# Kernel optimization log

Hardware: AMD Instinct MI355X
Metric: run time of the kernel (lower is better)

## Reference

```python
import jax, jax.numpy as jnp
import numpy as np

EMBED_DIM = 1024
NUM_HEADS = 16
NUM_GROUPS = 8
HEAD_DIM = EMBED_DIM // NUM_HEADS  # 64
HEADS_PER_GROUP = NUM_HEADS // NUM_GROUPS  # 2
B, S = 4, 2048


def setup_inputs() -> dict:
    key = jax.random.key(0)
    ks = jax.random.split(key, 9)
    init = lambda k, shape: jax.random.normal(k, shape, dtype=jnp.float32) * 0.02
    return {
        "x": jax.random.normal(ks[0], (B, S, EMBED_DIM), dtype=jnp.float32),
        "Wq": init(ks[1], (EMBED_DIM, NUM_GROUPS * HEAD_DIM)),
        "bq": jnp.zeros((NUM_GROUPS * HEAD_DIM,), jnp.float32),
        "Wk": init(ks[2], (EMBED_DIM, EMBED_DIM)),
        "bk": jnp.zeros((EMBED_DIM,), jnp.float32),
        "Wv": init(ks[3], (EMBED_DIM, EMBED_DIM)),
        "bv": jnp.zeros((EMBED_DIM,), jnp.float32),
        "Wo": init(ks[4], (EMBED_DIM, EMBED_DIM)),
        "bo": jnp.zeros((EMBED_DIM,), jnp.float32),
    }


def reference(x, Wq, bq, Wk, bk, Wv, bv, Wo, bo):
    b, s, _ = x.shape
    scale = HEAD_DIM ** -0.5
    # projections
    q = (x @ Wq + bq).reshape(b, s, NUM_GROUPS, HEAD_DIM).transpose(0, 2, 1, 3)   # [b,G,s,d]
    k = (x @ Wk + bk).reshape(b, s, NUM_HEADS, HEAD_DIM).transpose(0, 2, 1, 3)    # [b,H,s,d]
    v = (x @ Wv + bv).reshape(b, s, NUM_HEADS, HEAD_DIM).transpose(0, 2, 1, 3)    # [b,H,s,d]
    # repeat_interleave query groups up to full head count
    q = jnp.repeat(q, HEADS_PER_GROUP, axis=1)                                    # [b,H,s,d]
    scores = jnp.einsum("bhqd,bhkd->bhqk", q, k) * scale                          # [b,H,s,s]
    attn = jax.nn.softmax(scores, axis=-1)
    out = jnp.einsum("bhqk,bhkd->bhqd", attn, v)                                  # [b,H,s,d]
    out = out.transpose(0, 2, 1, 3).reshape(b, s, EMBED_DIM)
    return out @ Wo + bo
```

## Files before the change

kernel.cpp:

```cpp
#include <hip/hip_runtime.h>
#include <hip/hip_bf16.h>
#include <stdint.h>

typedef __bf16 bf16_t;
typedef __bf16 bf16x8 __attribute__((ext_vector_type(8)));
typedef __bf16 bf16x4 __attribute__((ext_vector_type(4)));
typedef float  f32x4  __attribute__((ext_vector_type(4)));
typedef float  f32x16 __attribute__((ext_vector_type(16)));
typedef unsigned int u32x2 __attribute__((ext_vector_type(2)));
typedef unsigned int u32x4 __attribute__((ext_vector_type(4)));

#define B_  4
#define S_  2048
#define H_  16
#define G_  8
#define D_  64

#define QSCALE 0.18033688011112042f
#define SM_BIAS -12.0f

__device__ __forceinline__ void gload_lds16(const bf16_t* g, void* l) {
  __builtin_amdgcn_global_load_lds((const __attribute__((address_space(1))) void*)g,
                                   (__attribute__((address_space(3))) void*)l,
                                   16, 0, 0);
}

__device__ __forceinline__ float fexp2(float x) {
  return __builtin_amdgcn_exp2f(x);
}

__device__ __forceinline__ unsigned cvt_pk(float a, float b) {
  unsigned r;
  asm("v_cvt_pk_bf16_f32 %0, %1, %2" : "=v"(r) : "v"(a), "v"(b));
  return r;
}

__device__ __forceinline__ float xhalf_add(float v) {
  u32x2 r = __builtin_amdgcn_permlane32_swap(__builtin_bit_cast(unsigned, v),
                                             __builtin_bit_cast(unsigned, v), false, false);
  return __builtin_bit_cast(float, r[0]) + __builtin_bit_cast(float, r[1]);
}

__global__ __launch_bounds__(256) void cast_x_kernel(const float* __restrict__ x,
                                                     bf16_t* __restrict__ y) {
  const size_t i = (size_t)blockIdx.x * blockDim.x + threadIdx.x;
  const f32x4* src = (const f32x4*)(x + i * 8);
  f32x4 a = src[0], b = src[1];
  bf16x8 o;
  o[0] = (bf16_t)a[0]; o[1] = (bf16_t)a[1]; o[2] = (bf16_t)a[2]; o[3] = (bf16_t)a[3];
  o[4] = (bf16_t)b[0]; o[5] = (bf16_t)b[1]; o[6] = (bf16_t)b[2]; o[7] = (bf16_t)b[3];
  *(bf16x8*)(y + i * 8) = o;
}

__global__ __launch_bounds__(256) void transpose_cast(const float* __restrict__ W,
                                                      bf16_t* __restrict__ WT,
                                                      int N, int rowOff) {
  __shared__ float tile[64][65];
  const int n0 = blockIdx.x * 64, k0 = blockIdx.y * 64;
  const int tx = threadIdx.x & 63, ty = threadIdx.x >> 6;
  #pragma unroll
  for (int r = ty; r < 64; r += 4)
    tile[r][tx] = W[(size_t)(k0 + r) * N + n0 + tx];
  __syncthreads();
  #pragma unroll
  for (int r = ty; r < 64; r += 4)
    WT[(size_t)(rowOff + n0 + r) * 1024 + k0 + tx] = (bf16_t)tile[tx][r];
}

template<int MODE>
__global__ __launch_bounds__(256) void gemm_bt(
    const bf16_t* __restrict__ A, const bf16_t* __restrict__ BT,
    const float* __restrict__ b0, const float* __restrict__ b1, const float* __restrict__ b2,
    bf16_t* __restrict__ qo, bf16_t* __restrict__ ko, bf16_t* __restrict__ vo,
    float* __restrict__ fout, int N) {
  __shared__ char lds[65536];
  const int tid  = threadIdx.x;
  const int wave = tid >> 6, lane = tid & 63;

  const int nwg  = gridDim.x * gridDim.y;
  const int cpx  = nwg >> 3;
  const int orig = blockIdx.y * gridDim.x + blockIdx.x;
  const int work = (orig & 7) * cpx + (orig >> 3);
  const int bx = work % gridDim.x, by = work / gridDim.x;

  const int bm = by * 128, bn = bx * 128;
  const int wm = (wave >> 1) * 64, wn = (wave & 1) * 64;
  const int l15 = lane & 15;

  const int sg = lane >> 3;
  const int sw = (lane & 7) ^ sg;
  const bf16_t* aSrc = A  + (size_t)(bm + sg) * 1024 + sw * 8;
  const bf16_t* bSrc = BT + (size_t)(bn + sg) * 1024 + sw * 8;

  const char* aAddr[2];
  const char* bAddr[2];
  #pragma unroll
  for (int ks = 0; ks < 2; ++ks) {
    const int slotx = ((ks * 4 + (lane >> 4)) ^ (l15 & 7)) << 4;
    aAddr[ks] = lds + (wm + l15) * 128 + slotx;
    bAddr[ks] = lds + 16384 + (wn + l15) * 128 + slotx;
  }

  f32x4 acc[4][4] = {};

  #define GSTAGE(kt_, SLOT_) do {                                              \
    char* dA_ = lds + (SLOT_) * 32768;                                         \
    char* dB_ = dA_ + 16384;                                                   \
    const int k0_ = (kt_) * 64;                                                \
    _Pragma("unroll")                                                          \
    for (int i_ = 0; i_ < 4; ++i_) {                                           \
      const int c_ = wave * 4 + i_;                                            \
      gload_lds16(aSrc + (size_t)c_ * 8 * 1024 + k0_, dA_ + c_ * 1024);        \
      gload_lds16(bSrc + (size_t)c_ * 8 * 1024 + k0_, dB_ + c_ * 1024);        \
    }                                                                          \
  } while (0)

  #define GWAIT0 do {                                                          \
    asm volatile("s_waitcnt vmcnt(0)" ::: "memory");                           \
    __builtin_amdgcn_s_barrier();                                              \
  } while (0)

  #define COMP(SLOT_) do {                                                     \
    _Pragma("unroll")                                                          \
    for (int ks = 0; ks < 2; ++ks) {                                           \
      bf16x8 af[4], bfr[4];                                                    \
      _Pragma("unroll")                                                        \
      for (int mt = 0; mt < 4; ++mt)                                           \
        af[mt] = *(const bf16x8*)(aAddr[ks] + mt * 2048 + (SLOT_) * 32768);    \
      _Pragma("unroll")                                                        \
      for (int nt = 0; nt < 4; ++nt)                                           \
        bfr[nt] = *(const bf16x8*)(bAddr[ks] + nt * 2048 + (SLOT_) * 32768);   \
      __builtin_amdgcn_s_setprio(1);                                           \
      _Pragma("unroll")                                                        \
      for (int mt = 0; mt < 4; ++mt)                                           \
        _Pragma("unroll")                                                      \
        for (int nt = 0; nt < 4; ++nt)                                         \
          acc[mt][nt] = __builtin_amdgcn_mfma_f32_16x16x32_bf16(af[mt], bfr[nt], acc[mt][nt], 0, 0, 0); \
      __builtin_amdgcn_s_setprio(0);                                           \
    }                                                                          \
  } while (0)

  GSTAGE(0, 0);
  GWAIT0;

  #pragma unroll 1
  for (int u = 0; u < 7; ++u) {
    GSTAGE(2 * u + 1, 1); COMP(0); GWAIT0;
    GSTAGE(2 * u + 2, 0); COMP(1); GWAIT0;
  }
  GSTAGE(15, 1); COMP(0); GWAIT0;
  COMP(1);

  #undef GSTAGE
  #undef GWAIT0
  #undef COMP

  if constexpr (MODE == 0) {
    if (bn >= 1536) {
      __syncthreads();
      #pragma unroll
      for (int nt = 0; nt < 4; ++nt) {
        const int nl = wn + nt * 16 + (lane & 15);
        const float bias = b2[bn - 1536 + nl];
        #pragma unroll
        for (int mt = 0; mt < 4; ++mt) {
          #pragma unroll
          for (int p = 0; p < 2; ++p) {
            const int ml = wm + mt * 16 + ((lane >> 4) << 2) + p * 2;
            unsigned u = cvt_pk(acc[mt][nt][p * 2] + bias, acc[mt][nt][p * 2 + 1] + bias);
            *(unsigned*)(lds + nl * 256 + ((((ml >> 3) ^ (nl & 15))) << 4) + (ml & 7) * 2) = u;
          }
        }
      }
      __syncthreads();
      const int bb = bm >> 11, sbase = bm & 2047;
      const int hv = (bn - 1536) >> 6;
      #pragma unroll
      for (int i = 0; i < 8; ++i) {
        const int nl = wave * 32 + i * 4 + (lane >> 4);
        const int mc = lane & 15;
        bf16x8 v = *(const bf16x8*)(lds + nl * 256 + ((mc ^ (nl & 15)) << 4));
        *(bf16x8*)(vo + (size_t)(bb * 16 + hv + (nl >> 6)) * 131072 +
                   (size_t)(nl & 63) * 2048 + sbase + mc * 8) = v;
      }
    } else {
      #pragma unroll
      for (int nt = 0; nt < 4; ++nt) {
        const int n = bn + wn + nt * 16 + (lane & 15);
        float bias; int region, hh, dd;
        if (n < 512) { region = 0; bias = b0[n];       hh = n >> 6;         dd = n & 63; }
        else         { region = 1; bias = b1[n - 512]; hh = (n - 512) >> 6; dd = (n - 512) & 63; }
        #pragma unroll
        for (int mt = 0; mt < 4; ++mt) {
          #pragma unroll
          for (int r = 0; r < 4; ++r) {
            const int m  = bm + wm + mt * 16 + ((lane >> 4) << 2) + r;
            const int bb = m >> 11, s = m & 2047;
            const float val = acc[mt][nt][r] + bias;
            if (region == 0)
              qo[(size_t)(bb * 8 + hh) * 131072 + s * 64 + dd] = (bf16_t)(val * QSCALE);
            else
              ko[(size_t)(bb * 16 + hh) * 131072 + s * 64 + dd] = (bf16_t)val;
          }
        }
      }
    }
  } else {
    #pragma unroll
    for (int nt = 0; nt < 4; ++nt) {
      const int n = bn + wn + nt * 16 + (lane & 15);
      const float bias = b0[n];
      #pragma unroll
      for (int mt = 0; mt < 4; ++mt) {
        #pragma unroll
        for (int r = 0; r < 4; ++r) {
          const int m = bm + wm + mt * 16 + ((lane >> 4) << 2) + r;
          fout[(size_t)m * 1024 + n] = acc[mt][nt][r] + bias;
        }
      }
    }
  }
}

__global__ __launch_bounds__(256, 2) void attn_kernel(
    const bf16_t* __restrict__ Q, const bf16_t* __restrict__ K,
    const bf16_t* __restrict__ Vt, bf16_t* __restrict__ O) {
  __shared__ char lds[49152];

  const int tid  = threadIdx.x;
  const int wave = tid >> 6, lane = tid & 63;
  const int bh = blockIdx.x;
  const int b = bh >> 4, h = bh & 15, g = h >> 1;
  const int qb = blockIdx.y * 256 + wave * 64;
  const int ql = lane & 31, hi = lane >> 5;
  const int swz = (ql & 7);

  const bf16_t* Qb = Q + ((size_t)(b * G_ + g) * S_ + qb) * D_;
  bf16x8 qf[2][4];
  #pragma unroll
  for (int qg = 0; qg < 2; ++qg)
    #pragma unroll
    for (int ks = 0; ks < 4; ++ks)
      qf[qg][ks] = *(const bf16x8*)(Qb + (size_t)(qg * 32 + ql) * D_ + ks * 16 + hi * 8);

  const char* ab[4];
  #pragma unroll
  for (int i = 0; i < 4; ++i)
    ab[i] = lds + ql * 128 + ((((i << 1) | hi) ^ swz) << 4);

  const int sg = lane >> 3, sw = (lane & 7) ^ sg;
  const int c = wave * 2;
  const bf16_t* kS = K  + (size_t)(b * H_ + h) * S_ * D_ + (size_t)(c * 8 + sg) * D_ + sw * 8;
  const bf16_t* vS = Vt + (size_t)(b * H_ + h) * D_ * S_ + (size_t)(c * 8 + sg) * S_ + sw * 8;

  #define STAGE(t_, SLOT_) do {                                                \
    char* nB = lds + (SLOT_) * 16384;                                          \
    const size_t koff_ = (size_t)(t_) * 64 * D_;                               \
    const size_t voff_ = (size_t)(t_) * 64;                                    \
    gload_lds16(kS + koff_,                 nB + c * 1024);                    \
    gload_lds16(kS + koff_ + 8 * D_,        nB + (c + 1) * 1024);              \
    gload_lds16(vS + voff_,                 nB + 8192 + c * 1024);             \
    gload_lds16(vS + voff_ + 8 * S_,        nB + 8192 + (c + 1) * 1024);       \
  } while (0)

  #define WAIT4 asm volatile("s_waitcnt vmcnt(4)" ::: "memory")
  #define WAIT0 asm volatile("s_waitcnt vmcnt(0)" ::: "memory")

  #define TILE(t_, SLOT_, WAITER_, DOSTAGE_) do {                              \
    WAITER_;                                                                   \
    __builtin_amdgcn_s_barrier();                                              \
    bf16x8 kf[2][4];                                                           \
    _Pragma("unroll")                                                          \
    for (int kg = 0; kg < 2; ++kg)                                             \
      _Pragma("unroll")                                                        \
      for (int ks = 0; ks < 4; ++ks)                                           \
        kf[kg][ks] = *(const bf16x8*)(ab[ks] + kg * 4096 + (SLOT_) * 16384);   \
    u32x4 pf[2][4];                                                            \
    _Pragma("unroll")                                                          \
    for (int qg = 0; qg < 2; ++qg) {                                           \
      f32x16 sc[2];                                                            \
      __builtin_amdgcn_s_setprio(1);                                           \
      sc[0] = __builtin_amdgcn_mfma_f32_32x32x16_bf16(kf[0][0], qf[qg][0], biasv, 0, 0, 0); \
      sc[1] = __builtin_amdgcn_mfma_f32_32x32x16_bf16(kf[1][0], qf[qg][0], biasv, 0, 0, 0); \
      _Pragma("unroll")                                                        \
      for (int ks = 1; ks < 4; ++ks) {                                         \
        sc[0] = __builtin_amdgcn_mfma_f32_32x32x16_bf16(kf[0][ks], qf[qg][ks], sc[0], 0, 0, 0); \
        sc[1] = __builtin_amdgcn_mfma_f32_32x32x16_bf16(kf[1][ks], qf[qg][ks], sc[1], 0, 0, 0); \
      }                                                                        \
      __builtin_amdgcn_s_setprio(0);                                           \
      _Pragma("unroll")                                                        \
      for (int kg = 0; kg < 2; ++kg)                                           \
        _Pragma("unroll")                                                      \
        for (int r = 0; r < 16; ++r)                                           \
          sc[kg][r] = fexp2(sc[kg][r]);                                        \
      lacc[qg] += sc[0];                                                       \
      lacc[qg] += sc[1];                                                       \
      _Pragma("unroll")                                                        \
      for (int kg = 0; kg < 2; ++kg) {                                         \
        _Pragma("unroll")                                                      \
        for (int k2 = 0; k2 < 2; ++k2) {                                       \
          unsigned u0 = cvt_pk(sc[kg][8 * k2 + 0], sc[kg][8 * k2 + 1]);        \
          unsigned u1 = cvt_pk(sc[kg][8 * k2 + 2], sc[kg][8 * k2 + 3]);        \
          unsigned u2 = cvt_pk(sc[kg][8 * k2 + 4], sc[kg][8 * k2 + 5]);        \
          unsigned u3 = cvt_pk(sc[kg][8 * k2 + 6], sc[kg][8 * k2 + 7]);        \
          u32x2 rA = __builtin_amdgcn_permlane32_swap(u0, u2, false, false);   \
          u32x2 rB = __builtin_amdgcn_permlane32_swap(u1, u3, false, false);   \
          u32x4 w; w[0] = rA[0]; w[1] = rB[0]; w[2] = rA[1]; w[3] = rB[1];     \
          pf[qg][kg * 2 + k2] = w;                                             \
        }                                                                      \
      }                                                                        \
    }                                                                          \
    __builtin_amdgcn_s_setprio(1);                                             \
    _Pragma("unroll")                                                          \
    for (int dg = 0; dg < 2; ++dg)                                             \
      _Pragma("unroll")                                                        \
      for (int s4 = 0; s4 < 4; ++s4) {                                         \
        bf16x8 vf = *(const bf16x8*)(ab[s4] + 8192 + dg * 4096 + (SLOT_) * 16384); \
        oacc[0][dg] = __builtin_amdgcn_mfma_f32_32x32x16_bf16(                 \
            vf, __builtin_bit_cast(bf16x8, pf[0][s4]), oacc[0][dg], 0, 0, 0);  \
        oacc[1][dg] = __builtin_amdgcn_mfma_f32_32x32x16_bf16(                 \
            vf, __builtin_bit_cast(bf16x8, pf[1][s4]), oacc[1][dg], 0, 0, 0);  \
      }                                                                        \
    __builtin_amdgcn_s_setprio(0);                                             \
    if (DOSTAGE_) STAGE((t_) + 2, ((SLOT_) + 2) % 3);                          \
  } while (0)

  STAGE(0, 0);
  STAGE(1, 1);

  f32x16 biasv;
  #pragma unroll
  for (int r = 0; r < 16; ++r) biasv[r] = SM_BIAS;

  f32x16 oacc[2][2] = {};
  f32x16 lacc[2] = {};

  #pragma unroll 1
  for (int u = 0; u < 10; ++u) {
    const int t0 = u * 3;
    TILE(t0,     0, WAIT4, 1);
    TILE(t0 + 1, 1, WAIT4, 1);
    TILE(t0 + 2, 2, WAIT4, 1);
  }
  TILE(30, 0, WAIT4, 0);
  TILE(31, 1, WAIT0, 0);

  #undef TILE
  #undef WAIT4
  #undef WAIT0
  #undef STAGE

  #pragma unroll
  for (int qg = 0; qg < 2; ++qg) {
    float l0 = (lacc[qg][0] + lacc[qg][8])  + (lacc[qg][1] + lacc[qg][9]);
    float l1 = (lacc[qg][2] + lacc[qg][10]) + (lacc[qg][3] + lacc[qg][11]);
    float l2 = (lacc[qg][4] + lacc[qg][12]) + (lacc[qg][5] + lacc[qg][13]);
    float l3 = (lacc[qg][6] + lacc[qg][14]) + (lacc[qg][7] + lacc[qg][15]);
    float lst = (l0 + l1) + (l2 + l3);
    lst = xhalf_add(lst);

    const int qrow = qb + qg * 32 + ql;
    const float inv = 1.f / lst;
    bf16_t* ob = O + ((size_t)(b * S_ + qrow) * H_ + h) * D_;
    #pragma unroll
    for (int dg = 0; dg < 2; ++dg) {
      #pragma unroll
      for (int rq = 0; rq < 4; ++rq) {
        bf16x4 o4;
        #pragma unroll
        for (int i = 0; i < 4; ++i)
          o4[i] = (bf16_t)(oacc[qg][dg][rq * 4 + i] * inv);
        *(bf16x4*)(ob + dg * 32 + rq * 8 + hi * 4) = o4;
      }
    }
  }
}

extern "C" void kernel_launch(void* const* d_in, const int* in_sizes, int n_in,
                              void* d_out, int out_size, void* d_ws, size_t ws_size,
                              hipStream_t stream) {
  const float* x  = (const float*)d_in[0];
  const float* Wq = (const float*)d_in[1];
  const float* bq = (const float*)d_in[2];
  const float* Wk = (const float*)d_in[3];
  const float* bk = (const float*)d_in[4];
  const float* Wv = (const float*)d_in[5];
  const float* bv = (const float*)d_in[6];
  const float* Wo = (const float*)d_in[7];
  const float* bo = (const float*)d_in[8];
  (void)in_sizes; (void)n_in; (void)out_size; (void)ws_size;

  char* ws = (char*)d_ws;
  bf16_t* xb  = (bf16_t*)(ws);
  bf16_t* WT  = (bf16_t*)(ws + (16u << 20));
  bf16_t* WoT = (bf16_t*)(ws + (22u << 20));
  bf16_t* q   = (bf16_t*)(ws + (24u << 20));
  bf16_t* kk  = (bf16_t*)(ws + (32u << 20));
  bf16_t* vT  = (bf16_t*)(ws + (48u << 20));
  bf16_t* ao  = (bf16_t*)(ws + (64u << 20));

  cast_x_kernel<<<4096, 256, 0, stream>>>(x, xb);
  transpose_cast<<<dim3(8, 16),  256, 0, stream>>>(Wq, WT, 512, 0);
  transpose_cast<<<dim3(16, 16), 256, 0, stream>>>(Wk, WT, 1024, 512);
  transpose_cast<<<dim3(16, 16), 256, 0, stream>>>(Wv, WT, 1024, 1536);
  transpose_cast<<<dim3(16, 16), 256, 0, stream>>>(Wo, WoT, 1024, 0);
  gemm_bt<0><<<dim3(20, 64), 256, 0, stream>>>(xb, WT, bq, bk, bv, q, kk, vT, nullptr, 2560);
  attn_kernel<<<dim3(64, 8), 256, 0, stream>>>(q, kk, vT, ao);
  gemm_bt<1><<<dim3(8, 64), 256, 0, stream>>>(ao, WoT, bo, nullptr, nullptr, nullptr,
                                              nullptr, nullptr, (float*)d_out, 1024);
}
```

Baseline: 180.3 us.

## Switch attention K/V pipeline to double-buffered two-tile stages with one barrier

```diff
diff --git a/kernel.cpp b/kernel.cpp
--- a/kernel.cpp
+++ b/kernel.cpp
@@ -225,7 +225,7 @@
 __global__ __launch_bounds__(256, 2) void attn_kernel(
     const bf16_t* __restrict__ Q, const bf16_t* __restrict__ K,
     const bf16_t* __restrict__ Vt, bf16_t* __restrict__ O) {
-  __shared__ char lds[49152];
+  __shared__ char lds[65536];
 
   const int tid  = threadIdx.x;
   const int wave = tid >> 6, lane = tid & 63;
@@ -253,28 +253,32 @@
   const bf16_t* kS = K  + (size_t)(b * H_ + h) * S_ * D_ + (size_t)(c * 8 + sg) * D_ + sw * 8;
   const bf16_t* vS = Vt + (size_t)(b * H_ + h) * D_ * S_ + (size_t)(c * 8 + sg) * S_ + sw * 8;
 
-  #define STAGE(t_, SLOT_) do {                                                \
-    char* nB = lds + (SLOT_) * 16384;                                          \
+  #define STAGE2(t_, H_) do {                                                  \
+    char* nB = lds + (H_) * 32768;                                             \
     const size_t koff_ = (size_t)(t_) * 64 * D_;                               \
     const size_t voff_ = (size_t)(t_) * 64;                                    \
-    gload_lds16(kS + koff_,                 nB + c * 1024);                    \
-    gload_lds16(kS + koff_ + 8 * D_,        nB + (c + 1) * 1024);              \
-    gload_lds16(vS + voff_,                 nB + 8192 + c * 1024);             \
-    gload_lds16(vS + voff_ + 8 * S_,        nB + 8192 + (c + 1) * 1024);       \
-  } while (0)
-
-  #define WAIT4 asm volatile("s_waitcnt vmcnt(4)" ::: "memory")
-  #define WAIT0 asm volatile("s_waitcnt vmcnt(0)" ::: "memory")
-
-  #define TILE(t_, SLOT_, WAITER_, DOSTAGE_) do {                              \
-    WAITER_;                                                                   \
+    gload_lds16(kS + koff_,                    nB + c * 1024);                 \
+    gload_lds16(kS + koff_ + 8 * D_,           nB + (c + 1) * 1024);           \
+    gload_lds16(vS + voff_,                    nB + 8192 + c * 1024);          \
+    gload_lds16(vS + voff_ + 8 * S_,           nB + 8192 + (c + 1) * 1024);    \
+    gload_lds16(kS + koff_ + 64 * D_,          nB + 16384 + c * 1024);         \
+    gload_lds16(kS + koff_ + 64 * D_ + 8 * D_, nB + 16384 + (c + 1) * 1024);   \
+    gload_lds16(vS + voff_ + 64,               nB + 24576 + c * 1024);         \
+    gload_lds16(vS + voff_ + 64 + 8 * S_,      nB + 24576 + (c + 1) * 1024);   \
+  } while (0)
+
+  #define WB do {                                                              \
+    asm volatile("s_waitcnt vmcnt(0)" ::: "memory");                           \
     __builtin_amdgcn_s_barrier();                                              \
+  } while (0)
+
+  #define TILE(BASE_) do {                                                     \
     bf16x8 kf[2][4];                                                           \
     _Pragma("unroll")                                                          \
     for (int kg = 0; kg < 2; ++kg)                                             \
       _Pragma("unroll")                                                        \
       for (int ks = 0; ks < 4; ++ks)                                           \
-        kf[kg][ks] = *(const bf16x8*)(ab[ks] + kg * 4096 + (SLOT_) * 16384);   \
+        kf[kg][ks] = *(const bf16x8*)(ab[ks] + kg * 4096 + (BASE_));           \
     u32x4 pf[2][4];                                                            \
     _Pragma("unroll")                                                          \
     for (int qg = 0; qg < 2; ++qg) {                                           \
@@ -315,18 +319,14 @@
     for (int dg = 0; dg < 2; ++dg)                                             \
       _Pragma("unroll")                                                        \
       for (int s4 = 0; s4 < 4; ++s4) {                                         \
-        bf16x8 vf = *(const bf16x8*)(ab[s4] + 8192 + dg * 4096 + (SLOT_) * 16384); \
+        bf16x8 vf = *(const bf16x8*)(ab[s4] + 8192 + dg * 4096 + (BASE_));     \
         oacc[0][dg] = __builtin_amdgcn_mfma_f32_32x32x16_bf16(                 \
             vf, __builtin_bit_cast(bf16x8, pf[0][s4]), oacc[0][dg], 0, 0, 0);  \
         oacc[1][dg] = __builtin_amdgcn_mfma_f32_32x32x16_bf16(                 \
             vf, __builtin_bit_cast(bf16x8, pf[1][s4]), oacc[1][dg], 0, 0, 0);  \
       }                                                                        \
     __builtin_amdgcn_s_setprio(0);                                             \
-    if (DOSTAGE_) STAGE((t_) + 2, ((SLOT_) + 2) % 3);                          \
-  } while (0)
-
-  STAGE(0, 0);
-  STAGE(1, 1);
+  } while (0)
 
   f32x16 biasv;
   #pragma unroll
@@ -335,20 +335,22 @@
   f32x16 oacc[2][2] = {};
   f32x16 lacc[2] = {};
 
+  STAGE2(0, 0);
+  WB;
+
   #pragma unroll 1
-  for (int u = 0; u < 10; ++u) {
-    const int t0 = u * 3;
-    TILE(t0,     0, WAIT4, 1);
-    TILE(t0 + 1, 1, WAIT4, 1);
-    TILE(t0 + 2, 2, WAIT4, 1);
+  for (int u = 0; u < 15; ++u) {
+    const int Hc = u & 1;
+    STAGE2(2 * u + 2, Hc ^ 1);
+    if (Hc == 0) { TILE(0);     TILE(16384); }
+    else         { TILE(32768); TILE(49152); }
+    WB;
   }
-  TILE(30, 0, WAIT4, 0);
-  TILE(31, 1, WAIT0, 0);
+  TILE(32768); TILE(49152);
 
   #undef TILE
-  #undef WAIT4
-  #undef WAIT0
-  #undef STAGE
+  #undef WB
+  #undef STAGE2
 
   #pragma unroll
   for (int qg = 0; qg < 2; ++qg) {
```

Result: slower. 328.2 us (+82.1%).

## Load K/V fragments directly from global memory instead of LDS triple buffering

Applied to the files above, without the earlier changes.

```diff
diff --git a/kernel.cpp b/kernel.cpp
--- a/kernel.cpp
+++ b/kernel.cpp
@@ -6,6 +6,7 @@
 typedef __bf16 bf16x8 __attribute__((ext_vector_type(8)));
 typedef __bf16 bf16x4 __attribute__((ext_vector_type(4)));
 typedef float  f32x4  __attribute__((ext_vector_type(4)));
+typedef float  f32x8  __attribute__((ext_vector_type(8)));
 typedef float  f32x16 __attribute__((ext_vector_type(16)));
 typedef unsigned int u32x2 __attribute__((ext_vector_type(2)));
 typedef unsigned int u32x4 __attribute__((ext_vector_type(4)));
@@ -225,15 +226,12 @@
 __global__ __launch_bounds__(256, 2) void attn_kernel(
     const bf16_t* __restrict__ Q, const bf16_t* __restrict__ K,
     const bf16_t* __restrict__ Vt, bf16_t* __restrict__ O) {
-  __shared__ char lds[49152];
-
   const int tid  = threadIdx.x;
   const int wave = tid >> 6, lane = tid & 63;
   const int bh = blockIdx.x;
   const int b = bh >> 4, h = bh & 15, g = h >> 1;
   const int qb = blockIdx.y * 256 + wave * 64;
   const int ql = lane & 31, hi = lane >> 5;
-  const int swz = (ql & 7);
 
   const bf16_t* Qb = Q + ((size_t)(b * G_ + g) * S_ + qb) * D_;
   bf16x8 qf[2][4];
@@ -243,120 +241,100 @@
     for (int ks = 0; ks < 4; ++ks)
       qf[qg][ks] = *(const bf16x8*)(Qb + (size_t)(qg * 32 + ql) * D_ + ks * 16 + hi * 8);
 
-  const char* ab[4];
-  #pragma unroll
-  for (int i = 0; i < 4; ++i)
-    ab[i] = lds + ql * 128 + ((((i << 1) | hi) ^ swz) << 4);
-
-  const int sg = lane >> 3, sw = (lane & 7) ^ sg;
-  const int c = wave * 2;
-  const bf16_t* kS = K  + (size_t)(b * H_ + h) * S_ * D_ + (size_t)(c * 8 + sg) * D_ + sw * 8;
-  const bf16_t* vS = Vt + (size_t)(b * H_ + h) * D_ * S_ + (size_t)(c * 8 + sg) * S_ + sw * 8;
-
-  #define STAGE(t_, SLOT_) do {                                                \
-    char* nB = lds + (SLOT_) * 16384;                                          \
-    const size_t koff_ = (size_t)(t_) * 64 * D_;                               \
-    const size_t voff_ = (size_t)(t_) * 64;                                    \
-    gload_lds16(kS + koff_,                 nB + c * 1024);                    \
-    gload_lds16(kS + koff_ + 8 * D_,        nB + (c + 1) * 1024);              \
-    gload_lds16(vS + voff_,                 nB + 8192 + c * 1024);             \
-    gload_lds16(vS + voff_ + 8 * S_,        nB + 8192 + (c + 1) * 1024);       \
-  } while (0)
-
-  #define WAIT4 asm volatile("s_waitcnt vmcnt(4)" ::: "memory")
-  #define WAIT0 asm volatile("s_waitcnt vmcnt(0)" ::: "memory")
-
-  #define TILE(t_, SLOT_, WAITER_, DOSTAGE_) do {                              \
-    WAITER_;                                                                   \
-    __builtin_amdgcn_s_barrier();                                              \
-    bf16x8 kf[2][4];                                                           \
-    _Pragma("unroll")                                                          \
-    for (int kg = 0; kg < 2; ++kg)                                             \
-      _Pragma("unroll")                                                        \
-      for (int ks = 0; ks < 4; ++ks)                                           \
-        kf[kg][ks] = *(const bf16x8*)(ab[ks] + kg * 4096 + (SLOT_) * 16384);   \
-    u32x4 pf[2][4];                                                            \
-    _Pragma("unroll")                                                          \
-    for (int qg = 0; qg < 2; ++qg) {                                           \
-      f32x16 sc[2];                                                            \
-      __builtin_amdgcn_s_setprio(1);                                           \
-      sc[0] = __builtin_amdgcn_mfma_f32_32x32x16_bf16(kf[0][0], qf[qg][0], biasv, 0, 0, 0); \
-      sc[1] = __builtin_amdgcn_mfma_f32_32x32x16_bf16(kf[1][0], qf[qg][0], biasv, 0, 0, 0); \
-      _Pragma("unroll")                                                        \
-      for (int ks = 1; ks < 4; ++ks) {                                         \
-        sc[0] = __builtin_amdgcn_mfma_f32_32x32x16_bf16(kf[0][ks], qf[qg][ks], sc[0], 0, 0, 0); \
-        sc[1] = __builtin_amdgcn_mfma_f32_32x32x16_bf16(kf[1][ks], qf[qg][ks], sc[1], 0, 0, 0); \
-      }                                                                        \
-      __builtin_amdgcn_s_setprio(0);                                           \
-      _Pragma("unroll")                                                        \
-      for (int kg = 0; kg < 2; ++kg)                                           \
-        _Pragma("unroll")                                                      \
-        for (int r = 0; r < 16; ++r)                                           \
-          sc[kg][r] = fexp2(sc[kg][r]);                                        \
-      lacc[qg] += sc[0];                                                       \
-      lacc[qg] += sc[1];                                                       \
-      _Pragma("unroll")                                                        \
-      for (int kg = 0; kg < 2; ++kg) {                                         \
-        _Pragma("unroll")                                                      \
-        for (int k2 = 0; k2 < 2; ++k2) {                                       \
-          unsigned u0 = cvt_pk(sc[kg][8 * k2 + 0], sc[kg][8 * k2 + 1]);        \
-          unsigned u1 = cvt_pk(sc[kg][8 * k2 + 2], sc[kg][8 * k2 + 3]);        \
-          unsigned u2 = cvt_pk(sc[kg][8 * k2 + 4], sc[kg][8 * k2 + 5]);        \
-          unsigned u3 = cvt_pk(sc[kg][8 * k2 + 6], sc[kg][8 * k2 + 7]);        \
-          u32x2 rA = __builtin_amdgcn_permlane32_swap(u0, u2, false, false);   \
-          u32x2 rB = __builtin_amdgcn_permlane32_swap(u1, u3, false, false);   \
-          u32x4 w; w[0] = rA[0]; w[1] = rB[0]; w[2] = rA[1]; w[3] = rB[1];     \
-          pf[qg][kg * 2 + k2] = w;                                             \
-        }                                                                      \
-      }                                                                        \
-    }                                                                          \
-    __builtin_amdgcn_s_setprio(1);                                             \
-    _Pragma("unroll")                                                          \
-    for (int dg = 0; dg < 2; ++dg)                                             \
-      _Pragma("unroll")                                                        \
-      for (int s4 = 0; s4 < 4; ++s4) {                                         \
-        bf16x8 vf = *(const bf16x8*)(ab[s4] + 8192 + dg * 4096 + (SLOT_) * 16384); \
-        oacc[0][dg] = __builtin_amdgcn_mfma_f32_32x32x16_bf16(                 \
-            vf, __builtin_bit_cast(bf16x8, pf[0][s4]), oacc[0][dg], 0, 0, 0);  \
-        oacc[1][dg] = __builtin_amdgcn_mfma_f32_32x32x16_bf16(                 \
-            vf, __builtin_bit_cast(bf16x8, pf[1][s4]), oacc[1][dg], 0, 0, 0);  \
-      }                                                                        \
-    __builtin_amdgcn_s_setprio(0);                                             \
-    if (DOSTAGE_) STAGE((t_) + 2, ((SLOT_) + 2) % 3);                          \
-  } while (0)
-
-  STAGE(0, 0);
-  STAGE(1, 1);
+  const bf16_t* kp  = K  + (size_t)(b * H_ + h) * S_ * D_ + (size_t)ql * D_ + hi * 8;
+  const bf16_t* vp0 = Vt + (size_t)(b * H_ + h) * D_ * S_ + (size_t)ql * S_ + hi * 8;
+  const bf16_t* vp1 = vp0 + (size_t)32 * S_;
 
   f32x16 biasv;
   #pragma unroll
   for (int r = 0; r < 16; ++r) biasv[r] = SM_BIAS;
 
   f32x16 oacc[2][2] = {};
-  f32x16 lacc[2] = {};
+  f32x8  lacc[2] = {};
 
   #pragma unroll 1
-  for (int u = 0; u < 10; ++u) {
-    const int t0 = u * 3;
-    TILE(t0,     0, WAIT4, 1);
-    TILE(t0 + 1, 1, WAIT4, 1);
-    TILE(t0 + 2, 2, WAIT4, 1);
-  }
-  TILE(30, 0, WAIT4, 0);
-  TILE(31, 1, WAIT0, 0);
-
-  #undef TILE
-  #undef WAIT4
-  #undef WAIT0
-  #undef STAGE
+  for (int t = 0; t < 32; ++t) {
+    const bf16_t* kt = kp + (size_t)t * 64 * D_;
+    bf16x8 kf[2][4];
+    #pragma unroll
+    for (int kg = 0; kg < 2; ++kg)
+      #pragma unroll
+      for (int ks = 0; ks < 4; ++ks)
+        kf[kg][ks] = *(const bf16x8*)(kt + kg * 32 * D_ + ks * 16);
+
+    bf16x8 vf0[4], vf1[4];
+    {
+      const bf16_t* vt0 = vp0 + (size_t)t * 64;
+      const bf16_t* vt1 = vp1 + (size_t)t * 64;
+      #pragma unroll
+      for (int s4 = 0; s4 < 4; ++s4) {
+        vf0[s4] = *(const bf16x8*)(vt0 + s4 * 16);
+        vf1[s4] = *(const bf16x8*)(vt1 + s4 * 16);
+      }
+    }
+
+    u32x4 pf[2][4];
+    #pragma unroll
+    for (int qg = 0; qg < 2; ++qg) {
+      f32x16 sc[2];
+      __builtin_amdgcn_s_setprio(1);
+      sc[0] = __builtin_amdgcn_mfma_f32_32x32x16_bf16(kf[0][0], qf[qg][0], biasv, 0, 0, 0);
+      sc[1] = __builtin_amdgcn_mfma_f32_32x32x16_bf16(kf[1][0], qf[qg][0], biasv, 0, 0, 0);
+      #pragma unroll
+      for (int ks = 1; ks < 4; ++ks) {
+        sc[0] = __builtin_amdgcn_mfma_f32_32x32x16_bf16(kf[0][ks], qf[qg][ks], sc[0], 0, 0, 0);
+        sc[1] = __builtin_amdgcn_mfma_f32_32x32x16_bf16(kf[1][ks], qf[qg][ks], sc[1], 0, 0, 0);
+      }
+      __builtin_amdgcn_s_setprio(0);
+
+      #pragma unroll
+      for (int kg = 0; kg < 2; ++kg)
+        #pragma unroll
+        for (int r = 0; r < 16; ++r)
+          sc[kg][r] = fexp2(sc[kg][r]);
+
+      {
+        f32x16 s_ = sc[0] + sc[1];
+        #pragma unroll
+        for (int r = 0; r < 8; ++r)
+          lacc[qg][r] += s_[r] + s_[r + 8];
+      }
+
+      #pragma unroll
+      for (int kg = 0; kg < 2; ++kg) {
+        #pragma unroll
+        for (int k2 = 0; k2 < 2; ++k2) {
+          unsigned u0 = cvt_pk(sc[kg][8 * k2 + 0], sc[kg][8 * k2 + 1]);
+          unsigned u1 = cvt_pk(sc[kg][8 * k2 + 2], sc[kg][8 * k2 + 3]);
+          unsigned u2 = cvt_pk(sc[kg][8 * k2 + 4], sc[kg][8 * k2 + 5]);
+          unsigned u3 = cvt_pk(sc[kg][8 * k2 + 6], sc[kg][8 * k2 + 7]);
+          u32x2 rA = __builtin_amdgcn_permlane32_swap(u0, u2, false, false);
+          u32x2 rB = __builtin_amdgcn_permlane32_swap(u1, u3, false, false);
+          u32x4 w; w[0] = rA[0]; w[1] = rB[0]; w[2] = rA[1]; w[3] = rB[1];
+          pf[qg][kg * 2 + k2] = w;
+        }
+      }
+    }
+
+    __builtin_amdgcn_s_setprio(1);
+    #pragma unroll
+    for (int dg = 0; dg < 2; ++dg)
+      #pragma unroll
+      for (int s4 = 0; s4 < 4; ++s4) {
+        bf16x8 vfr = (dg == 0) ? vf0[s4] : vf1[s4];
+        oacc[0][dg] = __builtin_amdgcn_mfma_f32_32x32x16_bf16(
+            vfr, __builtin_bit_cast(bf16x8, pf[0][s4]), oacc[0][dg], 0, 0, 0);
+        oacc[1][dg] = __builtin_amdgcn_mfma_f32_32x32x16_bf16(
+            vfr, __builtin_bit_cast(bf16x8, pf[1][s4]), oacc[1][dg], 0, 0, 0);
+      }
+    __builtin_amdgcn_s_setprio(0);
+  }
 
   #pragma unroll
   for (int qg = 0; qg < 2; ++qg) {
-    float l0 = (lacc[qg][0] + lacc[qg][8])  + (lacc[qg][1] + lacc[qg][9]);
-    float l1 = (lacc[qg][2] + lacc[qg][10]) + (lacc[qg][3] + lacc[qg][11]);
-    float l2 = (lacc[qg][4] + lacc[qg][12]) + (lacc[qg][5] + lacc[qg][13]);
-    float l3 = (lacc[qg][6] + lacc[qg][14]) + (lacc[qg][7] + lacc[qg][15]);
-    float lst = (l0 + l1) + (l2 + l3);
+    float l0 = (lacc[qg][0] + lacc[qg][4]) + (lacc[qg][1] + lacc[qg][5]);
+    float l1 = (lacc[qg][2] + lacc[qg][6]) + (lacc[qg][3] + lacc[qg][7]);
+    float lst = l0 + l1;
     lst = xhalf_add(lst);
 
     const int qrow = qb + qg * 32 + ql;
```

Result: slower. 235.4 us (+30.6%).
